# Performance work log

Measured on AMD Instinct MI355X. Metric: run time of the kernel, lower is better.

The kernel has to match this reference:

```python
import jax, jax.numpy as jnp
import numpy as np

N_PER_G = 18
GRAPHS = 4096
N = GRAPHS * N_PER_G            # 73728 nodes
E = GRAPHS * N_PER_G * (N_PER_G - 1)  # 1253376 edges (fully connected per graph)
F_IN = 1536                     # sfreq * timestep
EPS = 1e-5
SLOPE = 0.01


def _lrelu(v):
    return jnp.where(v >= 0, v, SLOPE * v)


def setup_inputs() -> dict:
    key = jax.random.key(0)
    ks = jax.random.split(key, 32)
    # node features
    x = jax.random.normal(ks[0], (N, F_IN), dtype=jnp.float32)
    # fully-connected edges within each 18-node graph
    src, dst = np.meshgrid(np.arange(N_PER_G), np.arange(N_PER_G), indexing='ij')
    m = src != dst
    src, dst = src[m], dst[m]                      # [306]
    offs = (np.arange(GRAPHS) * N_PER_G)[:, None]
    row = (offs + src[None, :]).reshape(-1)
    col = (offs + dst[None, :]).reshape(-1)
    edge_index = jnp.asarray(np.stack([row, col]), dtype=jnp.int32)  # [2,E]
    edge_weight = jax.random.uniform(ks[1], (E,), dtype=jnp.float32)
    batch = jnp.asarray(np.arange(N) // N_PER_G, dtype=jnp.int32)

    def lin(k, fi, fo):
        kw, kb = jax.random.split(k)
        s = 1.0 / np.sqrt(fi)
        W = jax.random.uniform(kw, (fi, fo), jnp.float32, -s, s)
        b = jax.random.uniform(kb, (fo,), jnp.float32, -s, s)
        return W, b

    def bn(k, f):
        k1, k2 = jax.random.split(k)
        g = jnp.ones((f,), jnp.float32)
        be = jnp.zeros((f,), jnp.float32)
        rm = jax.random.normal(k1, (f,), jnp.float32) * 0.1
        rv = jax.random.uniform(k2, (f,), jnp.float32) + 0.5
        return g, be, rm, rv

    W1, b1 = lin(ks[2], F_IN, 32)
    W2, b2 = lin(ks[3], 32, 64)
    W3, b3 = lin(ks[4], 64, 128)
    g1, be1, rm1, rv1 = bn(ks[5], 32)
    g2, be2, rm2, rv2 = bn(ks[6], 64)
    g3, be3, rm3, rv3 = bn(ks[7], 128)
    fW1, fb1 = lin(ks[8], 128, 64)
    fW2, fb2 = lin(ks[9], 64, 32)
    fW3, fb3 = lin(ks[10], 32, 16)
    fW4, fb4 = lin(ks[11], 16, 1)

    return dict(x=x, edge_index=edge_index, edge_weight=edge_weight, batch=batch,
                W1=W1, b1=b1, g1=g1, be1=be1, rm1=rm1, rv1=rv1,
                W2=W2, b2=b2, g2=g2, be2=be2, rm2=rm2, rv2=rv2,
                W3=W3, b3=b3, g3=g3, be3=be3, rm3=rm3, rv3=rv3,
                fW1=fW1, fb1=fb1, fW2=fW2, fb2=fb2,
                fW3=fW3, fb3=fb3, fW4=fW4, fb4=fb4)


def _gcn_norm(edge_index, edge_weight):
    # add self loops (weight 1), symmetric normalization (PyG GCNConv, improved=False)
    row = jnp.concatenate([edge_index[0], jnp.arange(N, dtype=edge_index.dtype)])
    col = jnp.concatenate([edge_index[1], jnp.arange(N, dtype=edge_index.dtype)])
    w = jnp.concatenate([edge_weight, jnp.ones((N,), edge_weight.dtype)])
    deg = jax.ops.segment_sum(w, col, num_segments=N)
    dinv = jnp.where(deg > 0, jax.lax.rsqrt(jnp.maximum(deg, 1e-30)), 0.0)
    norm = dinv[row] * w * dinv[col]
    return row, col, norm


def _gcn(x, W, b, row, col, norm):
    h = x @ W                                       # [N, Fout]
    out = jax.ops.segment_sum(norm[:, None] * h[row], col, num_segments=N)
    return out + b


def _bn(h, g, be, rm, rv):
    return (h - rm) * jax.lax.rsqrt(rv + EPS) * g + be


def reference(x, edge_index, edge_weight, batch,
              W1, b1, g1, be1, rm1, rv1,
              W2, b2, g2, be2, rm2, rv2,
              W3, b3, g3, be3, rm3, rv3,
              fW1, fb1, fW2, fb2, fW3, fb3, fW4, fb4):
    row, col, norm = _gcn_norm(edge_index, edge_weight)
    h = _lrelu(_bn(_gcn(x, W1, b1, row, col, norm), g1, be1, rm1, rv1))
    h = _lrelu(_bn(_gcn(h, W2, b2, row, col, norm), g2, be2, rm2, rv2))
    h = _lrelu(_bn(_gcn(h, W3, b3, row, col, norm), g3, be3, rm3, rv3))
    # global mean pool over graphs
    sums = jax.ops.segment_sum(h, batch, num_segments=GRAPHS)
    cnt = jax.ops.segment_sum(jnp.ones((N,), h.dtype), batch, num_segments=GRAPHS)
    h = sums / jnp.maximum(cnt, 1.0)[:, None]       # [G,128]
    # MLP head (dropout = identity in eval)
    h = _lrelu(h @ fW1 + fb1)
    h = _lrelu(h @ fW2 + fb2)
    h = _lrelu(h @ fW3 + fb3)
    h = h @ fW4 + fb4
    return h.squeeze(-1)                            # [G]
```

## Files before the change

kernel.cpp:

```cpp
#include <hip/hip_runtime.h>
#include <stdint.h>

#define GRAPHS 4096
#define NPG 18
#define EPERG 306
#define FIN 1536
#define BN_EPS 1e-5f
#define SLOPE 0.01f

using short8  = __attribute__((ext_vector_type(8))) short;
using ushort8 = __attribute__((ext_vector_type(8))) unsigned short;
using f32x4   = __attribute__((ext_vector_type(4))) float;
using f32x16  = __attribute__((ext_vector_type(16))) float;

__device__ __forceinline__ unsigned short f2bf(float f) {
  unsigned u = __builtin_bit_cast(unsigned, f);
  u += 0x7fffu + ((u >> 16) & 1u);
  return (unsigned short)(u >> 16);
}

__global__ void prep_kernel(const float* __restrict__ W1,
    const float* __restrict__ b1, const float* __restrict__ g1,
    const float* __restrict__ be1, const float* __restrict__ rm1, const float* __restrict__ rv1,
    const float* __restrict__ b2, const float* __restrict__ g2,
    const float* __restrict__ be2, const float* __restrict__ rm2, const float* __restrict__ rv2,
    const float* __restrict__ b3, const float* __restrict__ g3,
    const float* __restrict__ be3, const float* __restrict__ rm3, const float* __restrict__ rv3,
    unsigned short* __restrict__ w1frag, float* __restrict__ ab) {
  const int tid = threadIdx.x;
  if (blockIdx.x < 24) {
    int slot = blockIdx.x * 256 + tid;
    int L  = slot & 63;
    int ks = slot >> 6;
    int n  = L & 31;
    int kb = ks * 16 + ((L >> 5) << 3);
    ushort8 v;
#pragma unroll
    for (int j = 0; j < 8; ++j) v[j] = f2bf(W1[(kb + j) * 32 + n]);
    *((ushort8*)w1frag + slot) = v;
  } else {
    if (tid < 32) {
      float a = g1[tid] * rsqrtf(rv1[tid] + BN_EPS);
      ab[tid] = a; ab[32 + tid] = (b1[tid] - rm1[tid]) * a + be1[tid];
    }
    if (tid < 64) {
      float a = g2[tid] * rsqrtf(rv2[tid] + BN_EPS);
      ab[64 + tid] = a; ab[128 + tid] = (b2[tid] - rm2[tid]) * a + be2[tid];
    }
    if (tid < 128) {
      float a = g3[tid] * rsqrtf(rv3[tid] + BN_EPS);
      ab[192 + tid] = a; ab[320 + tid] = (b3[tid] - rm3[tid]) * a + be3[tid];
    }
  }
}

__global__ __launch_bounds__(256, 4) void gcn_fused(
    const float* __restrict__ x, const float* __restrict__ ew,
    const unsigned short* __restrict__ w1frag, const float* __restrict__ ab,
    const float* __restrict__ W2, const float* __restrict__ W3,
    const float* __restrict__ fW1, const float* __restrict__ fb1,
    const float* __restrict__ fW2, const float* __restrict__ fb2,
    const float* __restrict__ fW3, const float* __restrict__ fb3,
    const float* __restrict__ fW4, const float* __restrict__ fb4,
    float* __restrict__ out) {
  const int g    = blockIdx.x;
  const int tid  = threadIdx.x;
  const int lane = tid & 63;
  const int wv   = tid >> 6;

  __shared__ float ew_s[EPERG];
  __shared__ float dinv_s[NPG];
  __shared__ float An[NPG][NPG + 1];
  __shared__ __align__(16) float Pb[NPG][132];
  __shared__ __align__(16) float Hb[NPG][132];
  __shared__ __align__(16) float pooled[128];
  __shared__ float m1[64];
  __shared__ float m2[32];
  __shared__ float m3[16];

  for (int i = tid; i < EPERG; i += 256) ew_s[i] = ew[g * EPERG + i];

  const int r  = lane & 31;
  const int kg = lane >> 5;
  const bool valid = (r < NPG);
  f32x16 acc;
#pragma unroll
  for (int q = 0; q < 16; ++q) acc[q] = 0.f;

  const float* __restrict__ xr =
      x + (size_t)g * NPG * FIN + (size_t)r * FIN + (kg << 3);
  const short8* __restrict__ wf = (const short8*)w1frag + lane;

#pragma unroll 2
  for (int ks = 0; ks < 24; ++ks) {
    const int kidx = wv * 24 + ks;
    float4 a0 = {0.f, 0.f, 0.f, 0.f}, a1 = {0.f, 0.f, 0.f, 0.f};
    if (valid) {
      a0 = *(const float4*)(xr + kidx * 16);
      a1 = *(const float4*)(xr + kidx * 16 + 4);
    }
    short8 af;
    af[0] = (short)f2bf(a0.x); af[1] = (short)f2bf(a0.y);
    af[2] = (short)f2bf(a0.z); af[3] = (short)f2bf(a0.w);
    af[4] = (short)f2bf(a1.x); af[5] = (short)f2bf(a1.y);
    af[6] = (short)f2bf(a1.z); af[7] = (short)f2bf(a1.w);
    short8 bf = wf[(size_t)kidx * 64];
    acc = __builtin_amdgcn_mfma_f32_32x32x16_bf16(af, bf, acc, 0, 0, 0);
  }

  float* HbF = &Hb[0][0];
#pragma unroll
  for (int q = 0; q < 16; ++q) {
    int rr = (q & 3) + ((q >> 2) << 3) + (kg << 2);
    if (rr < NPG) HbF[wv * 576 + rr * 32 + r] = acc[q];
  }
  __syncthreads();

  if (tid < NPG) {
    float deg = 1.0f;
#pragma unroll
    for (int j = 0; j < 17; ++j) {
      int s = j + (j >= tid);
      deg += ew_s[s * 17 + (tid - (tid > s ? 1 : 0))];
    }
    dinv_s[tid] = rsqrtf(deg);
  }
  for (int o = tid; o < NPG * 32; o += 256) {
    Pb[o >> 5][o & 31] = HbF[o] + HbF[576 + o] + HbF[1152 + o] + HbF[1728 + o];
  }
  __syncthreads();

  for (int o = tid; o < NPG * NPG; o += 256) {
    int d = o / NPG, s = o - d * NPG;
    float v;
    if (d == s) v = dinv_s[d] * dinv_s[d];
    else        v = dinv_s[s] * ew_s[s * 17 + (d - (d > s ? 1 : 0))] * dinv_s[d];
    An[d][s] = v;
  }
  __syncthreads();

  for (int o = tid; o < NPG * 32; o += 256) {
    int d = o >> 5, cc = o & 31;
    float s = 0.f;
#pragma unroll
    for (int ss = 0; ss < NPG; ++ss) s = fmaf(An[d][ss], Pb[ss][cc], s);
    float v = fmaf(s, ab[cc], ab[32 + cc]);
    Hb[d][cc] = v >= 0.f ? v : SLOPE * v;
  }
  __syncthreads();

  for (int o = tid; o < NPG * 32; o += 256) {
    int d = o >> 5, cc = o & 31;
    float s = 0.f;
#pragma unroll
    for (int ss = 0; ss < NPG; ++ss) s = fmaf(An[d][ss], Hb[ss][cc], s);
    Pb[d][cc] = s;
  }
  __syncthreads();

  {
    const int cc = tid & 63;
    const int rg = tid >> 6;
    float a2[5] = {0.f, 0.f, 0.f, 0.f, 0.f};
#pragma unroll
    for (int k4 = 0; k4 < 8; ++k4) {
      float w0 = W2[(k4 * 4 + 0) * 64 + cc];
      float w1 = W2[(k4 * 4 + 1) * 64 + cc];
      float w2 = W2[(k4 * 4 + 2) * 64 + cc];
      float w3 = W2[(k4 * 4 + 3) * 64 + cc];
#pragma unroll
      for (int i = 0; i < 5; ++i) {
        int rr = rg + 4 * i;
        if (rr < NPG) {
          float4 a = *(const float4*)(&Pb[rr][k4 * 4]);
          a2[i] = fmaf(a.x, w0, fmaf(a.y, w1, fmaf(a.z, w2, fmaf(a.w, w3, a2[i]))));
        }
      }
    }
#pragma unroll
    for (int i = 0; i < 5; ++i) {
      int rr = rg + 4 * i;
      if (rr < NPG) {
        float v = fmaf(a2[i], ab[64 + cc], ab[128 + cc]);
        Hb[rr][cc] = v >= 0.f ? v : SLOPE * v;
      }
    }
  }
  __syncthreads();

  for (int o = tid; o < NPG * 64; o += 256) {
    int d = o >> 6, cc = o & 63;
    float s = 0.f;
#pragma unroll
    for (int ss = 0; ss < NPG; ++ss) s = fmaf(An[d][ss], Hb[ss][cc], s);
    Pb[d][cc] = s;
  }
  __syncthreads();

  {
    const int cc = tid & 127;
    const int rg = tid >> 7;
    float a3[9];
#pragma unroll
    for (int i = 0; i < 9; ++i) a3[i] = 0.f;
#pragma unroll
    for (int k4 = 0; k4 < 16; ++k4) {
      float w0 = W3[(k4 * 4 + 0) * 128 + cc];
      float w1 = W3[(k4 * 4 + 1) * 128 + cc];
      float w2 = W3[(k4 * 4 + 2) * 128 + cc];
      float w3 = W3[(k4 * 4 + 3) * 128 + cc];
#pragma unroll
      for (int i = 0; i < 9; ++i) {
        float4 a = *(const float4*)(&Pb[rg + 2 * i][k4 * 4]);
        a3[i] = fmaf(a.x, w0, fmaf(a.y, w1, fmaf(a.z, w2, fmaf(a.w, w3, a3[i]))));
      }
    }
#pragma unroll
    for (int i = 0; i < 9; ++i) {
      int rr = rg + 2 * i;
      float v = fmaf(a3[i], ab[192 + cc], ab[320 + cc]);
      Hb[rr][cc] = v >= 0.f ? v : SLOPE * v;
    }
  }
  __syncthreads();

  if (tid < 128) {
    float s = 0.f;
#pragma unroll
    for (int d = 0; d < NPG; ++d) s += Hb[d][tid];
    pooled[tid] = s * (1.0f / 18.0f);
  }
  __syncthreads();
  if (tid < 64) {
    float s = fb1[tid];
#pragma unroll
    for (int k4 = 0; k4 < 32; ++k4) {
      float4 p = *(const float4*)(&pooled[k4 * 4]);
      s = fmaf(p.x, fW1[(k4 * 4 + 0) * 64 + tid], s);
      s = fmaf(p.y, fW1[(k4 * 4 + 1) * 64 + tid], s);
      s = fmaf(p.z, fW1[(k4 * 4 + 2) * 64 + tid], s);
      s = fmaf(p.w, fW1[(k4 * 4 + 3) * 64 + tid], s);
    }
    m1[tid] = s >= 0.f ? s : SLOPE * s;
  }
  __syncthreads();
  if (tid < 32) {
    float s = fb2[tid];
#pragma unroll
    for (int k = 0; k < 64; ++k) s = fmaf(m1[k], fW2[k * 32 + tid], s);
    m2[tid] = s >= 0.f ? s : SLOPE * s;
  }
  __syncthreads();
  if (tid < 16) {
    float s = fb3[tid];
#pragma unroll
    for (int k = 0; k < 32; ++k) s = fmaf(m2[k], fW3[k * 16 + tid], s);
    m3[tid] = s >= 0.f ? s : SLOPE * s;
  }
  __syncthreads();
  if (tid == 0) {
    float s = fb4[0];
#pragma unroll
    for (int k = 0; k < 16; ++k) s = fmaf(m3[k], fW4[k], s);
    out[g] = s;
  }
}

extern "C" void kernel_launch(void* const* d_in, const int* in_sizes, int n_in,
                              void* d_out, int out_size, void* d_ws, size_t ws_size,
                              hipStream_t stream) {
  const float* x   = (const float*)d_in[0];
  const float* ew  = (const float*)d_in[2];
  const float* W1  = (const float*)d_in[4];
  const float* b1  = (const float*)d_in[5];
  const float* g1  = (const float*)d_in[6];
  const float* be1 = (const float*)d_in[7];
  const float* rm1 = (const float*)d_in[8];
  const float* rv1 = (const float*)d_in[9];
  const float* W2  = (const float*)d_in[10];
  const float* b2  = (const float*)d_in[11];
  const float* g2  = (const float*)d_in[12];
  const float* be2 = (const float*)d_in[13];
  const float* rm2 = (const float*)d_in[14];
  const float* rv2 = (const float*)d_in[15];
  const float* W3  = (const float*)d_in[16];
  const float* b3  = (const float*)d_in[17];
  const float* g3  = (const float*)d_in[18];
  const float* be3 = (const float*)d_in[19];
  const float* rm3 = (const float*)d_in[20];
  const float* rv3 = (const float*)d_in[21];
  const float* fW1 = (const float*)d_in[22];
  const float* fb1 = (const float*)d_in[23];
  const float* fW2 = (const float*)d_in[24];
  const float* fb2 = (const float*)d_in[25];
  const float* fW3 = (const float*)d_in[26];
  const float* fb3 = (const float*)d_in[27];
  const float* fW4 = (const float*)d_in[28];
  const float* fb4 = (const float*)d_in[29];

  unsigned short* w1frag = (unsigned short*)d_ws;
  float* ab   = (float*)((char*)d_ws + 98304);

  prep_kernel<<<25, 256, 0, stream>>>(W1, b1, g1, be1, rm1, rv1,
                                      b2, g2, be2, rm2, rv2,
                                      b3, g3, be3, rm3, rv3,
                                      w1frag, ab);
  gcn_fused<<<GRAPHS, 256, 0, stream>>>(x, ew, w1frag, ab, W2, W3, fW1,
                                        fb1, fW2, fb2, fW3, fb3, fW4, fb4,
                                        (float*)d_out);
}
```

Measured before the change: 709.0 us.

## Persistent blocks overlap next graph's X·W1 MFMA with current graph's GCN tail

Result: slower. 1.504 ms (+112.2%).

```diff
diff --git a/kernel.cpp b/kernel.cpp
--- a/kernel.cpp
+++ b/kernel.cpp
@@ -54,6 +54,48 @@
   }
 }
 
+struct Chunk { float4 a00, a01, a10, a11, a20, a21, a30, a31; };
+
+__device__ __forceinline__ void load_chunk(Chunk& ch, const float* __restrict__ xr,
+                                           int kb, bool valid) {
+  if (valid) {
+    ch.a00 = *(const float4*)(xr + (kb + 0) * 16);
+    ch.a01 = *(const float4*)(xr + (kb + 0) * 16 + 4);
+    ch.a10 = *(const float4*)(xr + (kb + 1) * 16);
+    ch.a11 = *(const float4*)(xr + (kb + 1) * 16 + 4);
+    ch.a20 = *(const float4*)(xr + (kb + 2) * 16);
+    ch.a21 = *(const float4*)(xr + (kb + 2) * 16 + 4);
+    ch.a30 = *(const float4*)(xr + (kb + 3) * 16);
+    ch.a31 = *(const float4*)(xr + (kb + 3) * 16 + 4);
+  }
+}
+
+__device__ __forceinline__ short8 pack_bf16(const float4& a0, const float4& a1) {
+  short8 af;
+  af[0] = (short)f2bf(a0.x); af[1] = (short)f2bf(a0.y);
+  af[2] = (short)f2bf(a0.z); af[3] = (short)f2bf(a0.w);
+  af[4] = (short)f2bf(a1.x); af[5] = (short)f2bf(a1.y);
+  af[6] = (short)f2bf(a1.z); af[7] = (short)f2bf(a1.w);
+  return af;
+}
+
+__device__ __forceinline__ void mfma_chunk(f32x16& acc, const Chunk& ch,
+                                           const short8* __restrict__ wf, int kb) {
+  acc = __builtin_amdgcn_mfma_f32_32x32x16_bf16(pack_bf16(ch.a00, ch.a01), wf[(size_t)(kb + 0) * 64], acc, 0, 0, 0);
+  acc = __builtin_amdgcn_mfma_f32_32x32x16_bf16(pack_bf16(ch.a10, ch.a11), wf[(size_t)(kb + 1) * 64], acc, 0, 0, 0);
+  acc = __builtin_amdgcn_mfma_f32_32x32x16_bf16(pack_bf16(ch.a20, ch.a21), wf[(size_t)(kb + 2) * 64], acc, 0, 0, 0);
+  acc = __builtin_amdgcn_mfma_f32_32x32x16_bf16(pack_bf16(ch.a30, ch.a31), wf[(size_t)(kb + 3) * 64], acc, 0, 0, 0);
+}
+
+__device__ __forceinline__ void spill_acc(float* HbF, int wv, int kg, int r,
+                                          const f32x16& acc) {
+#pragma unroll
+  for (int q = 0; q < 16; ++q) {
+    int rr = (q & 3) + ((q >> 2) << 3) + (kg << 2);
+    if (rr < NPG) HbF[wv * 576 + rr * 32 + r] = acc[q];
+  }
+}
+
 __global__ __launch_bounds__(256, 4) void gcn_fused(
     const float* __restrict__ x, const float* __restrict__ ew,
     const unsigned short* __restrict__ w1frag, const float* __restrict__ ab,
@@ -63,10 +105,13 @@
     const float* __restrict__ fW3, const float* __restrict__ fb3,
     const float* __restrict__ fW4, const float* __restrict__ fb4,
     float* __restrict__ out) {
-  const int g    = blockIdx.x;
+  const int bid  = blockIdx.x;
   const int tid  = threadIdx.x;
   const int lane = tid & 63;
   const int wv   = tid >> 6;
+  const int r    = lane & 31;
+  const int kg   = lane >> 5;
+  const bool valid = (r < NPG);
 
   __shared__ float ew_s[EPERG];
   __shared__ float dinv_s[NPG];
@@ -74,195 +119,227 @@
   __shared__ __align__(16) float Pb[NPG][132];
   __shared__ __align__(16) float Hb[NPG][132];
   __shared__ __align__(16) float pooled[128];
-  __shared__ float m1[64];
-  __shared__ float m2[32];
-  __shared__ float m3[16];
-
-  for (int i = tid; i < EPERG; i += 256) ew_s[i] = ew[g * EPERG + i];
-
-  const int r  = lane & 31;
-  const int kg = lane >> 5;
-  const bool valid = (r < NPG);
+  float* HbF = &Hb[0][0];
+
+  const short8* __restrict__ wf = (const short8*)w1frag + lane;
+
+  for (int i = tid; i < EPERG; i += 256) ew_s[i] = ew[(size_t)bid * EPERG + i];
+
   f32x16 acc;
 #pragma unroll
   for (int q = 0; q < 16; ++q) acc[q] = 0.f;
-
-  const float* __restrict__ xr =
-      x + (size_t)g * NPG * FIN + (size_t)r * FIN + (kg << 3);
-  const short8* __restrict__ wf = (const short8*)w1frag + lane;
-
-#pragma unroll 2
-  for (int ks = 0; ks < 24; ++ks) {
-    const int kidx = wv * 24 + ks;
-    float4 a0 = {0.f, 0.f, 0.f, 0.f}, a1 = {0.f, 0.f, 0.f, 0.f};
-    if (valid) {
-      a0 = *(const float4*)(xr + kidx * 16);
-      a1 = *(const float4*)(xr + kidx * 16 + 4);
-    }
-    short8 af;
-    af[0] = (short)f2bf(a0.x); af[1] = (short)f2bf(a0.y);
-    af[2] = (short)f2bf(a0.z); af[3] = (short)f2bf(a0.w);
-    af[4] = (short)f2bf(a1.x); af[5] = (short)f2bf(a1.y);
-    af[6] = (short)f2bf(a1.z); af[7] = (short)f2bf(a1.w);
-    short8 bf = wf[(size_t)kidx * 64];
-    acc = __builtin_amdgcn_mfma_f32_32x32x16_bf16(af, bf, acc, 0, 0, 0);
-  }
-
-  float* HbF = &Hb[0][0];
-#pragma unroll
-  for (int q = 0; q < 16; ++q) {
-    int rr = (q & 3) + ((q >> 2) << 3) + (kg << 2);
-    if (rr < NPG) HbF[wv * 576 + rr * 32 + r] = acc[q];
-  }
-  __syncthreads();
-
-  if (tid < NPG) {
-    float deg = 1.0f;
-#pragma unroll
-    for (int j = 0; j < 17; ++j) {
-      int s = j + (j >= tid);
-      deg += ew_s[s * 17 + (tid - (tid > s ? 1 : 0))];
-    }
-    dinv_s[tid] = rsqrtf(deg);
-  }
-  for (int o = tid; o < NPG * 32; o += 256) {
-    Pb[o >> 5][o & 31] = HbF[o] + HbF[576 + o] + HbF[1152 + o] + HbF[1728 + o];
-  }
-  __syncthreads();
-
-  for (int o = tid; o < NPG * NPG; o += 256) {
-    int d = o / NPG, s = o - d * NPG;
-    float v;
-    if (d == s) v = dinv_s[d] * dinv_s[d];
-    else        v = dinv_s[s] * ew_s[s * 17 + (d - (d > s ? 1 : 0))] * dinv_s[d];
-    An[d][s] = v;
-  }
-  __syncthreads();
-
-  for (int o = tid; o < NPG * 32; o += 256) {
-    int d = o >> 5, cc = o & 31;
-    float s = 0.f;
-#pragma unroll
-    for (int ss = 0; ss < NPG; ++ss) s = fmaf(An[d][ss], Pb[ss][cc], s);
-    float v = fmaf(s, ab[cc], ab[32 + cc]);
-    Hb[d][cc] = v >= 0.f ? v : SLOPE * v;
-  }
-  __syncthreads();
-
-  for (int o = tid; o < NPG * 32; o += 256) {
-    int d = o >> 5, cc = o & 31;
-    float s = 0.f;
-#pragma unroll
-    for (int ss = 0; ss < NPG; ++ss) s = fmaf(An[d][ss], Hb[ss][cc], s);
-    Pb[d][cc] = s;
-  }
-  __syncthreads();
+  Chunk ch;
+  ch.a00 = ch.a01 = ch.a10 = ch.a11 = float4{0.f, 0.f, 0.f, 0.f};
+  ch.a20 = ch.a21 = ch.a30 = ch.a31 = float4{0.f, 0.f, 0.f, 0.f};
 
   {
-    const int cc = tid & 63;
-    const int rg = tid >> 6;
-    float a2[5] = {0.f, 0.f, 0.f, 0.f, 0.f};
-#pragma unroll
-    for (int k4 = 0; k4 < 8; ++k4) {
-      float w0 = W2[(k4 * 4 + 0) * 64 + cc];
-      float w1 = W2[(k4 * 4 + 1) * 64 + cc];
-      float w2 = W2[(k4 * 4 + 2) * 64 + cc];
-      float w3 = W2[(k4 * 4 + 3) * 64 + cc];
-#pragma unroll
-      for (int i = 0; i < 5; ++i) {
-        int rr = rg + 4 * i;
+    const float* __restrict__ xr =
+        x + (size_t)bid * NPG * FIN + (size_t)r * FIN + (kg << 3);
+#pragma unroll 4
+    for (int ks = 0; ks < 24; ++ks) {
+      const int kidx = wv * 24 + ks;
+      float4 a0 = {0.f, 0.f, 0.f, 0.f}, a1 = {0.f, 0.f, 0.f, 0.f};
+      if (valid) {
+        a0 = *(const float4*)(xr + kidx * 16);
+        a1 = *(const float4*)(xr + kidx * 16 + 4);
+      }
+      acc = __builtin_amdgcn_mfma_f32_32x32x16_bf16(
+          pack_bf16(a0, a1), wf[(size_t)kidx * 64], acc, 0, 0, 0);
+    }
+  }
+  spill_acc(HbF, wv, kg, r, acc);
+#pragma unroll
+  for (int q = 0; q < 16; ++q) acc[q] = 0.f;
+
+#pragma unroll 1
+  for (int i = 0; i < 4; ++i) {
+    const int gi = bid + (i << 10);
+    const int gn = gi + 1024;
+    const bool pf = (i < 3);
+    const float* __restrict__ xrn =
+        x + (size_t)gn * NPG * FIN + (size_t)r * FIN + (kg << 3);
+
+    __syncthreads();
+
+    if (pf) load_chunk(ch, xrn, wv * 24 + 0, valid);
+    if (tid < NPG) {
+      float deg = 1.0f;
+#pragma unroll
+      for (int j = 0; j < 17; ++j) {
+        int s = j + (j >= tid);
+        deg += ew_s[s * 17 + (tid - (tid > s ? 1 : 0))];
+      }
+      dinv_s[tid] = rsqrtf(deg);
+    }
+    {
+      const f32x4* HbF4 = (const f32x4*)HbF;
+      for (int o4 = tid; o4 < 144; o4 += 256) {
+        f32x4 v = HbF4[o4];
+        v += HbF4[144 + o4];
+        v += HbF4[288 + o4];
+        v += HbF4[432 + o4];
+        *(f32x4*)&Pb[o4 >> 3][(o4 & 7) << 2] = v;
+      }
+    }
+    __syncthreads();
+
+    if (pf) { mfma_chunk(acc, ch, wf, wv * 24 + 0); load_chunk(ch, xrn, wv * 24 + 4, valid); }
+    for (int o = tid; o < NPG * NPG; o += 256) {
+      int d = o / NPG, s = o - d * NPG;
+      float v;
+      if (d == s) v = dinv_s[d] * dinv_s[d];
+      else        v = dinv_s[s] * ew_s[s * 17 + (d - (d > s ? 1 : 0))] * dinv_s[d];
+      An[d][s] = v;
+    }
+    __syncthreads();
+
+    if (pf) { mfma_chunk(acc, ch, wf, wv * 24 + 4); load_chunk(ch, xrn, wv * 24 + 8, valid); }
+    if (pf) for (int o = tid; o < EPERG; o += 256) ew_s[o] = ew[(size_t)gn * EPERG + o];
+    for (int o4 = tid; o4 < 144; o4 += 256) {
+      int d = o4 >> 3, cb = (o4 & 7) << 2;
+      f32x4 s = {0.f, 0.f, 0.f, 0.f};
+#pragma unroll
+      for (int ss = 0; ss < NPG; ++ss) {
+        float a = An[d][ss];
+        f32x4 p = *(const f32x4*)&Pb[ss][cb];
+        s[0] = fmaf(a, p[0], s[0]); s[1] = fmaf(a, p[1], s[1]);
+        s[2] = fmaf(a, p[2], s[2]); s[3] = fmaf(a, p[3], s[3]);
+      }
+#pragma unroll
+      for (int j = 0; j < 4; ++j) {
+        float v = fmaf(s[j], ab[cb + j], ab[32 + cb + j]);
+        s[j] = v >= 0.f ? v : SLOPE * v;
+      }
+      *(f32x4*)&Hb[d][cb] = s;
+    }
+    __syncthreads();
+
+    if (pf) { mfma_chunk(acc, ch, wf, wv * 24 + 8); load_chunk(ch, xrn, wv * 24 + 12, valid); }
+    for (int o4 = tid; o4 < 144; o4 += 256) {
+      int d = o4 >> 3, cb = (o4 & 7) << 2;
+      f32x4 s = {0.f, 0.f, 0.f, 0.f};
+#pragma unroll
+      for (int ss = 0; ss < NPG; ++ss) {
+        float a = An[d][ss];
+        f32x4 p = *(const f32x4*)&Hb[ss][cb];
+        s[0] = fmaf(a, p[0], s[0]); s[1] = fmaf(a, p[1], s[1]);
+        s[2] = fmaf(a, p[2], s[2]); s[3] = fmaf(a, p[3], s[3]);
+      }
+      *(f32x4*)&Pb[d][cb] = s;
+    }
+    __syncthreads();
+
+    if (pf) { mfma_chunk(acc, ch, wf, wv * 24 + 12); load_chunk(ch, xrn, wv * 24 + 16, valid); }
+    {
+      const int cc = tid & 63;
+      const int rg = tid >> 6;
+      float a2[5] = {0.f, 0.f, 0.f, 0.f, 0.f};
+#pragma unroll
+      for (int k4 = 0; k4 < 8; ++k4) {
+        float w0 = W2[(k4 * 4 + 0) * 64 + cc];
+        float w1 = W2[(k4 * 4 + 1) * 64 + cc];
+        float w2 = W2[(k4 * 4 + 2) * 64 + cc];
+        float w3 = W2[(k4 * 4 + 3) * 64 + cc];
+#pragma unroll
+        for (int ii = 0; ii < 5; ++ii) {
+          int rr = rg + 4 * ii;
+          if (rr < NPG) {
+            float4 a = *(const float4*)(&Pb[rr][k4 * 4]);
+            a2[ii] = fmaf(a.x, w0, fmaf(a.y, w1, fmaf(a.z, w2, fmaf(a.w, w3, a2[ii]))));
+          }
+        }
+      }
+#pragma unroll
+      for (int ii = 0; ii < 5; ++ii) {
+        int rr = rg + 4 * ii;
         if (rr < NPG) {
-          float4 a = *(const float4*)(&Pb[rr][k4 * 4]);
-          a2[i] = fmaf(a.x, w0, fmaf(a.y, w1, fmaf(a.z, w2, fmaf(a.w, w3, a2[i]))));
+          float v = fmaf(a2[ii], ab[64 + cc], ab[128 + cc]);
+          Hb[rr][cc] = v >= 0.f ? v : SLOPE * v;
         }
       }
     }
-#pragma unroll
-    for (int i = 0; i < 5; ++i) {
-      int rr = rg + 4 * i;
-      if (rr < NPG) {
-        float v = fmaf(a2[i], ab[64 + cc], ab[128 + cc]);
-        Hb[rr][cc] = v >= 0.f ? v : SLOPE * v;
-      }
-    }
-  }
-  __syncthreads();
-
-  for (int o = tid; o < NPG * 64; o += 256) {
-    int d = o >> 6, cc = o & 63;
-    float s = 0.f;
-#pragma unroll
-    for (int ss = 0; ss < NPG; ++ss) s = fmaf(An[d][ss], Hb[ss][cc], s);
-    Pb[d][cc] = s;
-  }
-  __syncthreads();
-
-  {
-    const int cc = tid & 127;
-    const int rg = tid >> 7;
-    float a3[9];
-#pragma unroll
-    for (int i = 0; i < 9; ++i) a3[i] = 0.f;
-#pragma unroll
-    for (int k4 = 0; k4 < 16; ++k4) {
-      float w0 = W3[(k4 * 4 + 0) * 128 + cc];
-      float w1 = W3[(k4 * 4 + 1) * 128 + cc];
-      float w2 = W3[(k4 * 4 + 2) * 128 + cc];
-      float w3 = W3[(k4 * 4 + 3) * 128 + cc];
-#pragma unroll
-      for (int i = 0; i < 9; ++i) {
-        float4 a = *(const float4*)(&Pb[rg + 2 * i][k4 * 4]);
-        a3[i] = fmaf(a.x, w0, fmaf(a.y, w1, fmaf(a.z, w2, fmaf(a.w, w3, a3[i]))));
-      }
-    }
-#pragma unroll
-    for (int i = 0; i < 9; ++i) {
-      int rr = rg + 2 * i;
-      float v = fmaf(a3[i], ab[192 + cc], ab[320 + cc]);
-      Hb[rr][cc] = v >= 0.f ? v : SLOPE * v;
-    }
-  }
-  __syncthreads();
-
-  if (tid < 128) {
-    float s = 0.f;
-#pragma unroll
-    for (int d = 0; d < NPG; ++d) s += Hb[d][tid];
-    pooled[tid] = s * (1.0f / 18.0f);
-  }
-  __syncthreads();
-  if (tid < 64) {
-    float s = fb1[tid];
-#pragma unroll
-    for (int k4 = 0; k4 < 32; ++k4) {
-      float4 p = *(const float4*)(&pooled[k4 * 4]);
-      s = fmaf(p.x, fW1[(k4 * 4 + 0) * 64 + tid], s);
-      s = fmaf(p.y, fW1[(k4 * 4 + 1) * 64 + tid], s);
-      s = fmaf(p.z, fW1[(k4 * 4 + 2) * 64 + tid], s);
-      s = fmaf(p.w, fW1[(k4 * 4 + 3) * 64 + tid], s);
-    }
-    m1[tid] = s >= 0.f ? s : SLOPE * s;
-  }
-  __syncthreads();
-  if (tid < 32) {
-    float s = fb2[tid];
-#pragma unroll
-    for (int k = 0; k < 64; ++k) s = fmaf(m1[k], fW2[k * 32 + tid], s);
-    m2[tid] = s >= 0.f ? s : SLOPE * s;
-  }
-  __syncthreads();
-  if (tid < 16) {
-    float s = fb3[tid];
-#pragma unroll
-    for (int k = 0; k < 32; ++k) s = fmaf(m2[k], fW3[k * 16 + tid], s);
-    m3[tid] = s >= 0.f ? s : SLOPE * s;
-  }
-  __syncthreads();
-  if (tid == 0) {
-    float s = fb4[0];
-#pragma unroll
-    for (int k = 0; k < 16; ++k) s = fmaf(m3[k], fW4[k], s);
-    out[g] = s;
+    __syncthreads();
+
+    if (pf) { mfma_chunk(acc, ch, wf, wv * 24 + 16); load_chunk(ch, xrn, wv * 24 + 20, valid); }
+    for (int o4 = tid; o4 < 288; o4 += 256) {
+      int d = o4 >> 4, cb = (o4 & 15) << 2;
+      f32x4 s = {0.f, 0.f, 0.f, 0.f};
+#pragma unroll
+      for (int ss = 0; ss < NPG; ++ss) {
+        float a = An[d][ss];
+        f32x4 p = *(const f32x4*)&Hb[ss][cb];
+        s[0] = fmaf(a, p[0], s[0]); s[1] = fmaf(a, p[1], s[1]);
+        s[2] = fmaf(a, p[2], s[2]); s[3] = fmaf(a, p[3], s[3]);
+      }
+      *(f32x4*)&Pb[d][cb] = s;
+    }
+    __syncthreads();
+
+    if (pf) mfma_chunk(acc, ch, wf, wv * 24 + 20);
+    {
+      const int cc = tid & 127;
+      const int rg = tid >> 7;
+      float a3[9];
+#pragma unroll
+      for (int ii = 0; ii < 9; ++ii) a3[ii] = 0.f;
+#pragma unroll
+      for (int k4 = 0; k4 < 16; ++k4) {
+        float w0 = W3[(k4 * 4 + 0) * 128 + cc];
+        float w1 = W3[(k4 * 4 + 1) * 128 + cc];
+        float w2 = W3[(k4 * 4 + 2) * 128 + cc];
+        float w3 = W3[(k4 * 4 + 3) * 128 + cc];
+#pragma unroll
+        for (int ii = 0; ii < 9; ++ii) {
+          float4 a = *(const float4*)(&Pb[rg + 2 * ii][k4 * 4]);
+          a3[ii] = fmaf(a.x, w0, fmaf(a.y, w1, fmaf(a.z, w2, fmaf(a.w, w3, a3[ii]))));
+        }
+      }
+#pragma unroll
+      for (int ii = 0; ii < 9; ++ii) {
+        float v = fmaf(a3[ii], ab[192 + cc], ab[320 + cc]);
+        Hb[rg + 2 * ii][cc] = v >= 0.f ? v : SLOPE * v;
+      }
+    }
+    __syncthreads();
+
+    if (tid < 128) {
+      float s = 0.f;
+#pragma unroll
+      for (int d = 0; d < NPG; ++d) s += Hb[d][tid];
+      pooled[tid] = s * (1.0f / 18.0f);
+    }
+    __syncthreads();
+
+    if (pf) {
+      spill_acc(HbF, wv, kg, r, acc);
+#pragma unroll
+      for (int q = 0; q < 16; ++q) acc[q] = 0.f;
+    }
+    if (wv == 3) {
+      const int L = lane;
+      float s1 = fb1[L];
+#pragma unroll
+      for (int k4 = 0; k4 < 32; ++k4) {
+        float4 p = *(const float4*)(&pooled[k4 * 4]);
+        s1 = fmaf(p.x, fW1[(k4 * 4 + 0) * 64 + L], s1);
+        s1 = fmaf(p.y, fW1[(k4 * 4 + 1) * 64 + L], s1);
+        s1 = fmaf(p.z, fW1[(k4 * 4 + 2) * 64 + L], s1);
+        s1 = fmaf(p.w, fW1[(k4 * 4 + 3) * 64 + L], s1);
+      }
+      s1 = s1 >= 0.f ? s1 : SLOPE * s1;
+      float s2 = fb2[L & 31];
+#pragma unroll
+      for (int k = 0; k < 64; ++k) s2 = fmaf(__shfl(s1, k), fW2[k * 32 + (L & 31)], s2);
+      s2 = s2 >= 0.f ? s2 : SLOPE * s2;
+      float s3 = fb3[L & 15];
+#pragma unroll
+      for (int k = 0; k < 32; ++k) s3 = fmaf(__shfl(s2, k), fW3[k * 16 + (L & 15)], s3);
+      s3 = s3 >= 0.f ? s3 : SLOPE * s3;
+      float s4 = fb4[0];
+#pragma unroll
+      for (int k = 0; k < 16; ++k) s4 = fmaf(__shfl(s3, k), fW4[k], s4);
+      if (L == 0) out[gi] = s4;
+    }
   }
 }
 
@@ -305,7 +382,7 @@
                                       b2, g2, be2, rm2, rv2,
                                       b3, g3, be3, rm3, rv3,
                                       w1frag, ab);
-  gcn_fused<<<GRAPHS, 256, 0, stream>>>(x, ew, w1frag, ab, W2, W3, fW1,
-                                        fb1, fW2, fb2, fW3, fb3, fW4, fb4,
-                                        (float*)d_out);
-}
+  gcn_fused<<<1024, 256, 0, stream>>>(x, ew, w1frag, ab, W2, W3, fW1,
+                                      fb1, fW2, fb2, fW3, fb3, fW4, fb4,
+                                      (float*)d_out);
+}
```

## Split MLP head into separate wave-per-graph kernel with LDS-staged weights

Applied to the files above, without the earlier changes.

After: 718.6 us. Within noise of the previous version (+1.4%).

```diff
diff --git a/kernel.cpp b/kernel.cpp
--- a/kernel.cpp
+++ b/kernel.cpp
@@ -58,11 +58,7 @@
     const float* __restrict__ x, const float* __restrict__ ew,
     const unsigned short* __restrict__ w1frag, const float* __restrict__ ab,
     const float* __restrict__ W2, const float* __restrict__ W3,
-    const float* __restrict__ fW1, const float* __restrict__ fb1,
-    const float* __restrict__ fW2, const float* __restrict__ fb2,
-    const float* __restrict__ fW3, const float* __restrict__ fb3,
-    const float* __restrict__ fW4, const float* __restrict__ fb4,
-    float* __restrict__ out) {
+    float* __restrict__ pooledg) {
   const int g    = blockIdx.x;
   const int tid  = threadIdx.x;
   const int lane = tid & 63;
@@ -73,10 +69,6 @@
   __shared__ float An[NPG][NPG + 1];
   __shared__ __align__(16) float Pb[NPG][132];
   __shared__ __align__(16) float Hb[NPG][132];
-  __shared__ __align__(16) float pooled[128];
-  __shared__ float m1[64];
-  __shared__ float m2[32];
-  __shared__ float m3[16];
 
   for (int i = tid; i < EPERG; i += 256) ew_s[i] = ew[g * EPERG + i];
 
@@ -228,42 +220,57 @@
     float s = 0.f;
 #pragma unroll
     for (int d = 0; d < NPG; ++d) s += Hb[d][tid];
-    pooled[tid] = s * (1.0f / 18.0f);
-  }
-  __syncthreads();
-  if (tid < 64) {
-    float s = fb1[tid];
-#pragma unroll
-    for (int k4 = 0; k4 < 32; ++k4) {
-      float4 p = *(const float4*)(&pooled[k4 * 4]);
-      s = fmaf(p.x, fW1[(k4 * 4 + 0) * 64 + tid], s);
-      s = fmaf(p.y, fW1[(k4 * 4 + 1) * 64 + tid], s);
-      s = fmaf(p.z, fW1[(k4 * 4 + 2) * 64 + tid], s);
-      s = fmaf(p.w, fW1[(k4 * 4 + 3) * 64 + tid], s);
-    }
-    m1[tid] = s >= 0.f ? s : SLOPE * s;
-  }
-  __syncthreads();
-  if (tid < 32) {
-    float s = fb2[tid];
-#pragma unroll
-    for (int k = 0; k < 64; ++k) s = fmaf(m1[k], fW2[k * 32 + tid], s);
-    m2[tid] = s >= 0.f ? s : SLOPE * s;
-  }
-  __syncthreads();
-  if (tid < 16) {
-    float s = fb3[tid];
-#pragma unroll
-    for (int k = 0; k < 32; ++k) s = fmaf(m2[k], fW3[k * 16 + tid], s);
-    m3[tid] = s >= 0.f ? s : SLOPE * s;
-  }
-  __syncthreads();
-  if (tid == 0) {
-    float s = fb4[0];
-#pragma unroll
-    for (int k = 0; k < 16; ++k) s = fmaf(m3[k], fW4[k], s);
-    out[g] = s;
-  }
+    pooledg[(size_t)g * 128 + tid] = s * (1.0f / 18.0f);
+  }
+}
+
+__global__ __launch_bounds__(256) void head_kernel(
+    const float* __restrict__ pooled,
+    const float* __restrict__ fW1, const float* __restrict__ fb1,
+    const float* __restrict__ fW2, const float* __restrict__ fb2,
+    const float* __restrict__ fW3, const float* __restrict__ fb3,
+    const float* __restrict__ fW4, const float* __restrict__ fb4,
+    float* __restrict__ out) {
+  const int tid  = threadIdx.x;
+  const int lane = tid & 63;
+  const int wv   = tid >> 6;
+
+  __shared__ __align__(16) float w1s[128 * 64];
+  __shared__ __align__(16) float w2s[64 * 32];
+  __shared__ __align__(16) float w3s[32 * 16];
+  __shared__ float w4s[16];
+
+  for (int i = tid; i < 128 * 64; i += 256) w1s[i] = fW1[i];
+  for (int i = tid; i < 64 * 32; i += 256)  w2s[i] = fW2[i];
+  for (int i = tid; i < 32 * 16; i += 256)  w3s[i] = fW3[i];
+  if (tid < 16) w4s[tid] = fW4[tid];
+  __syncthreads();
+
+  const int g = (blockIdx.x << 2) + wv;
+  const float p0 = pooled[(size_t)g * 128 + lane];
+  const float p1 = pooled[(size_t)g * 128 + 64 + lane];
+
+  float s1 = fb1[lane];
+#pragma unroll
+  for (int k = 0; k < 64; ++k) s1 = fmaf(__shfl(p0, k), w1s[k * 64 + lane], s1);
+#pragma unroll
+  for (int k = 0; k < 64; ++k) s1 = fmaf(__shfl(p1, k), w1s[(64 + k) * 64 + lane], s1);
+  s1 = s1 >= 0.f ? s1 : SLOPE * s1;
+
+  float s2 = fb2[lane & 31];
+#pragma unroll
+  for (int k = 0; k < 64; ++k) s2 = fmaf(__shfl(s1, k), w2s[k * 32 + (lane & 31)], s2);
+  s2 = s2 >= 0.f ? s2 : SLOPE * s2;
+
+  float s3 = fb3[lane & 15];
+#pragma unroll
+  for (int k = 0; k < 32; ++k) s3 = fmaf(__shfl(s2, k), w3s[k * 16 + (lane & 15)], s3);
+  s3 = s3 >= 0.f ? s3 : SLOPE * s3;
+
+  float s4 = fb4[0];
+#pragma unroll
+  for (int k = 0; k < 16; ++k) s4 = fmaf(__shfl(s3, k), w4s[k], s4);
+  if (lane == 0) out[g] = s4;
 }
 
 extern "C" void kernel_launch(void* const* d_in, const int* in_sizes, int n_in,
@@ -299,13 +306,14 @@
   const float* fb4 = (const float*)d_in[29];
 
   unsigned short* w1frag = (unsigned short*)d_ws;
-  float* ab   = (float*)((char*)d_ws + 98304);
+  float* ab     = (float*)((char*)d_ws + 98304);
+  float* pooled = (float*)((char*)d_ws + 102400);
 
   prep_kernel<<<25, 256, 0, stream>>>(W1, b1, g1, be1, rm1, rv1,
                                       b2, g2, be2, rm2, rv2,
                                       b3, g3, be3, rm3, rv3,
                                       w1frag, ab);
-  gcn_fused<<<GRAPHS, 256, 0, stream>>>(x, ew, w1frag, ab, W2, W3, fW1,
-                                        fb1, fW2, fb2, fW3, fb3, fW4, fb4,
-                                        (float*)d_out);
-}
+  gcn_fused<<<GRAPHS, 256, 0, stream>>>(x, ew, w1frag, ab, W2, W3, pooled);
+  head_kernel<<<1024, 256, 0, stream>>>(pooled, fW1, fb1, fW2, fb2,
+                                        fW3, fb3, fW4, fb4, (float*)d_out);
+}
```
